# Optimization experiments

Measured on AMD Instinct MI355X. Metric: run time of the kernel, lower is better.

The kernel has to match this reference:

```python
import jax, jax.numpy as jnp
import numpy as np
from jax.scipy.linalg import solve_triangular

DT = 0.1
LOG2PI = float(np.log(2.0 * np.pi))


def _mvn_ll(r, L):
    # r: (B, dz, K) residual, L: (dz, dz) lower-tri Cholesky of cov
    B_, dz, K = r.shape
    y = solve_triangular(L, r.transpose(1, 0, 2).reshape(dz, -1), lower=True)
    quad = jnp.sum(y * y, axis=0).reshape(B_, K)
    logdet = jnp.sum(jnp.log(jnp.diag(L)))
    return -0.5 * quad - logdet - 0.5 * dz * LOG2PI


def _diag_ll(r, std):
    # r: (B, dz, K), std: (dz,) -> (B, K)
    z = r / std[None, :, None]
    return -0.5 * jnp.sum(z * z, axis=1) - jnp.sum(jnp.log(std)) - 0.5 * r.shape[1] * LOG2PI


def _systematic_resample(log_w, key):
    # systematic resampling (aesmc style): stratified positions bucketized into cum weights
    B_, K = log_w.shape
    u0 = jax.random.uniform(key, (B_, 1))
    pos = (u0 + jnp.arange(K, dtype=log_w.dtype)) / K
    w = jax.nn.softmax(jax.lax.stop_gradient(log_w), axis=1)
    cw = jnp.cumsum(w, axis=1)
    cw = cw / cw[:, -1:]
    idx = jax.vmap(lambda c, p: jnp.searchsorted(c, p))(cw, pos)
    return jnp.clip(idx, 0, K - 1)


def _transition(z, v, m, n, Wu, h):
    # low-rank RNN prior: z'= (1-dt) z + dt m^T tanh(n z + Wu v + h); z: (B,dz,K), v: (B,du)
    pre = jnp.einsum('Nz,BzK->BNK', n, z) + (v @ Wu.T)[:, :, None] + h[None, :, None]
    return (1.0 - DT) * z + DT * jnp.einsum('Nz,BNK->BzK', m, jnp.tanh(pre))


def _kalman(var_z, var_x, B_obs):
    # precision-form optimal proposal (dim_x >= 4*dim_z branch)
    dz = var_z.shape[0]
    prec = jnp.diag(1.0 / var_z) + (B_obs / var_x[None, :]) @ B_obs.T
    var_Q = jnp.linalg.inv(prec)
    Kg = var_Q @ (B_obs / var_x[None, :])           # (dz, dx)
    one_min_alpha = jnp.eye(dz) - Kg @ B_obs.T      # (dz, dz)
    var_Q = 1e-8 * jnp.eye(dz) + 0.5 * (var_Q + var_Q.T)
    L = jnp.linalg.cholesky(var_Q)
    return Kg, one_min_alpha, L


def setup_inputs() -> dict:
    key = jax.random.key(0)
    ks = jax.random.split(key, 14)
    B_, dx, T = 128, 128, 512
    dz, du, dN, K = 16, 8, 512, 128
    inp = {
        'x': jax.random.normal(ks[0], (B_, dx, T), jnp.float32),
        'u': jax.random.normal(ks[1], (B_, du, T), jnp.float32),
        'R_z': 0.1 + 0.1 * jax.random.uniform(ks[2], (dz,), jnp.float32),
        'R_z_t0': 0.2 + 0.1 * jax.random.uniform(ks[3], (dz,), jnp.float32),
        'R_x': 0.3 + 0.2 * jax.random.uniform(ks[4], (dx,), jnp.float32),
        'B_obs': jax.random.normal(ks[5], (dz, dx), jnp.float32) / np.sqrt(dz),
        'Obs_bias': 0.1 * jax.random.normal(ks[6], (dx,), jnp.float32),
        'm': jax.random.normal(ks[7], (dN, dz), jnp.float32) / np.sqrt(dN),
        'n': jax.random.normal(ks[8], (dN, dz), jnp.float32) / np.sqrt(dz),
        'Wu': jax.random.normal(ks[9], (dN, du), jnp.float32) / np.sqrt(du),
        'h': 0.1 * jax.random.normal(ks[10], (dN,), jnp.float32),
        'W0': jax.random.normal(ks[11], (dz, du), jnp.float32) / np.sqrt(du),
        'b0': 0.1 * jax.random.normal(ks[12], (dz,), jnp.float32),
        'k': K,
    }
    return inp


def reference(x, u, R_z, R_z_t0, R_x, B_obs, Obs_bias, m, n, Wu, h, W0, b0, k):
    B_, dx, T = x.shape
    dz = R_z.shape[0]
    K = int(k)
    var_z = R_z ** 2 + 1e-8
    var_z0 = R_z_t0 ** 2 + 1e-8
    var_x = jnp.clip(R_x ** 2, 1e-8)
    std_x = jnp.clip(jnp.abs(R_x), 1e-4)
    std_z = jnp.sqrt(var_z)
    std_z0 = jnp.sqrt(var_z0)
    log_std_x_sum = jnp.sum(jnp.log(std_x))

    Kg0, oma0, L0 = _kalman(var_z0, var_x, B_obs)
    Kg, oma, L = _kalman(var_z, var_x, B_obs)
    base = jax.random.key(42)
    logk = jnp.log(jnp.asarray(K, x.dtype))

    def obs_ll(xt, Qz):
        mean_x = jnp.einsum('zx,BzK->BxK', B_obs, Qz) + Obs_bias[None, :, None]
        rx = (xt[:, :, None] - mean_x) / std_x[None, :, None]
        return -0.5 * jnp.sum(rx * rx, axis=1) - log_std_x_sum - 0.5 * dx * LOG2PI

    # t = 0: initial state from stimulus, Kalman optimal proposal
    prior_mean = (u[:, :, 0] @ W0.T + b0)[:, :, None] * jnp.ones((1, 1, K), x.dtype)
    mean_Q = jnp.einsum('zs,BsK->BzK', oma0, prior_mean) \
        + jnp.einsum('zx,Bx->Bz', Kg0, x[:, :, 0] - Obs_bias)[:, :, None]
    eps = jax.random.normal(jax.random.fold_in(base, 0), (B_, dz, K), x.dtype)
    Qz = mean_Q + jnp.einsum('zs,BsK->BzK', L0, eps)
    ll_qz = _mvn_ll(Qz - mean_Q, L0)
    ll_pz = _diag_ll(Qz - prior_mean, std_z0)
    ll_x = obs_ll(x[:, :, 0], Qz)
    log_w = ll_x + ll_pz - ll_qz
    elbo0 = jax.scipy.special.logsumexp(log_w, axis=-1) - logk

    x_tm = jnp.moveaxis(x[:, :, 1:], 2, 0)       # (T-1, B, dx)
    v_tm = jnp.moveaxis(u[:, :, :T - 1], 2, 0)   # v at step t is u[:,:,t-1]
    ts = jnp.arange(1, T)

    def step(carry, inp):
        Qz, log_w = carry
        xt, vt, t = inp
        k1, k2 = jax.random.split(jax.random.fold_in(base, t))
        idx = _systematic_resample(log_w, k1)
        Qz = jnp.take_along_axis(Qz, jnp.broadcast_to(idx[:, None, :], Qz.shape), axis=2)
        prior_mean = _transition(Qz, vt, m, n, Wu, h)
        mean_Q = jnp.einsum('zs,BsK->BzK', oma, prior_mean) \
            + jnp.einsum('zx,Bx->Bz', Kg, xt - Obs_bias)[:, :, None]
        eps = jax.random.normal(k2, Qz.shape, Qz.dtype)
        Qz_new = mean_Q + jnp.einsum('zs,BsK->BzK', L, eps)
        ll_qz = _mvn_ll(Qz_new - mean_Q, L)
        ll_pz = _diag_ll(Qz_new - prior_mean, std_z)
        ll_x = obs_ll(xt, Qz_new)
        log_w_new = ll_x + ll_pz - ll_qz
        return (Qz_new, log_w_new), jax.scipy.special.logsumexp(log_w_new, axis=-1) - logk

    (_, _), elbos = jax.lax.scan(step, (Qz, log_w), (x_tm, v_tm, ts))
    loss = -(elbo0 + jnp.sum(elbos, axis=0)) / T   # (B,) negative per-trial ELBO
    return loss
```

## Files before the change

kernel.cpp:

```cpp
#include <hip/hip_runtime.h>
#include <hip/hip_bf16.h>


#define WS_KG    0
#define WS_OMA   4096
#define WS_L     4608
#define WS_RSTDZ 5120
#define WS_RSTDX 5152
#define WS_CONST 5280

#define LOG2PI_F 1.8378770664093453f

typedef __attribute__((ext_vector_type(8))) short short8v;
typedef __attribute__((ext_vector_type(4))) float float4v;
typedef __attribute__((ext_vector_type(4))) unsigned uint4v;

#define MFMA32(a, b, c) \
  __builtin_amdgcn_mfma_f32_16x16x32_bf16((a), (b), (c), 0, 0, 0)

__device__ __forceinline__ unsigned rotl32(unsigned v, int r) {
  return (v << r) | (v >> (32 - r));
}

__device__ __forceinline__ void tf2x32(unsigned k0, unsigned k1,
                                       unsigned c0, unsigned c1,
                                       unsigned& o0, unsigned& o1) {
  unsigned ks2 = k0 ^ k1 ^ 0x1BD11BDAu;
  unsigned x0 = c0 + k0, x1 = c1 + k1;
#define TF_R4(ra, rb, rc, rd) \
  x0 += x1; x1 = rotl32(x1, ra); x1 ^= x0; \
  x0 += x1; x1 = rotl32(x1, rb); x1 ^= x0; \
  x0 += x1; x1 = rotl32(x1, rc); x1 ^= x0; \
  x0 += x1; x1 = rotl32(x1, rd); x1 ^= x0;
  TF_R4(13, 15, 26, 6)  x0 += k1;  x1 += ks2 + 1u;
  TF_R4(17, 29, 16, 24) x0 += ks2; x1 += k0 + 2u;
  TF_R4(13, 15, 26, 6)  x0 += k0;  x1 += k1 + 3u;
  TF_R4(17, 29, 16, 24) x0 += k1;  x1 += ks2 + 4u;
  TF_R4(13, 15, 26, 6)  x0 += ks2; x1 += k0 + 5u;
#undef TF_R4
  o0 = x0; o1 = x1;
}

__device__ __forceinline__ float erfinv_f(float x) {
  float w = -log1pf(-x * x);
  float p;
  if (w < 5.0f) {
    w -= 2.5f;
    p = 2.81022636e-08f;
    p = fmaf(p, w, 3.43273939e-07f);
    p = fmaf(p, w, -3.5233877e-06f);
    p = fmaf(p, w, -4.39150654e-06f);
    p = fmaf(p, w, 0.00021858087f);
    p = fmaf(p, w, -0.00125372503f);
    p = fmaf(p, w, -0.00417768164f);
    p = fmaf(p, w, 0.246640727f);
    p = fmaf(p, w, 1.50140941f);
  } else {
    w = sqrtf(w) - 3.0f;
    p = -0.000200214257f;
    p = fmaf(p, w, 0.000100950558f);
    p = fmaf(p, w, 0.00134934322f);
    p = fmaf(p, w, -0.00367342844f);
    p = fmaf(p, w, 0.00573950773f);
    p = fmaf(p, w, -0.0076224613f);
    p = fmaf(p, w, 0.00943887047f);
    p = fmaf(p, w, 1.00167406f);
    p = fmaf(p, w, 2.83297682f);
  }
  return p * x;
}

__device__ __forceinline__ float normal_from_bits(unsigned bits) {
  float f = __uint_as_float((bits >> 9) | 0x3f800000u) - 1.0f;
  const float lo = -0.99999994f;
  float uu = fmaxf(lo, fmaf(f, 2.0f, lo));
  return 1.41421354f * erfinv_f(uu);
}

__device__ __forceinline__ float tanh_fast2(float d) {
  float e = __expf(d);
  return 1.0f - 2.0f * __builtin_amdgcn_rcpf(e + 1.0f);
}

__device__ __forceinline__ short f2bf(float f) {
  unsigned u = __float_as_uint(f);
  unsigned r = (u + 0x7fffu + ((u >> 16) & 1u)) >> 16;
  return (short)r;
}

__device__ __forceinline__ unsigned packbf(float a, float b) {
  return (unsigned)(unsigned short)f2bf(a) |
         ((unsigned)(unsigned short)f2bf(b) << 16);
}

__device__ __forceinline__ unsigned cvtpk(float a, float b) {
  unsigned r;
  asm("v_cvt_pk_bf16_f32 %0, %1, %2" : "=v"(r) : "v"(a), "v"(b));
  return r;
}

__device__ __forceinline__ short8v mk8(unsigned a, unsigned b,
                                       unsigned c, unsigned d) {
  uint4v u = {a, b, c, d};
  return __builtin_bit_cast(short8v, u);
}

__global__ void precomp_kernel(const float* __restrict__ Rz,
                               const float* __restrict__ Rz0,
                               const float* __restrict__ Rx,
                               const float* __restrict__ Bobs,
                               float* __restrict__ ws) {
  __shared__ float svarx[128];
  __shared__ float svarz[16];
  __shared__ float sprec[16][16];
  __shared__ float saug[16][32];
  __shared__ float svq[16][16];
  __shared__ float sLm[16][16];
  __shared__ float skg[16][128];
  const int tid = threadIdx.x;

  if (tid < 128) {
    float r = Rx[tid];
    svarx[tid] = fmaxf(r * r, 1e-8f);
    ws[WS_RSTDX + tid] = 1.0f / fmaxf(fabsf(r), 1e-4f);
  }
  if (tid == 0) {
    float a = 0.0f;
    for (int xx = 0; xx < 128; ++xx) a += logf(fmaxf(fabsf(Rx[xx]), 1e-4f));
    ws[WS_CONST + 0] = -a - 0.5f * 128.0f * LOG2PI_F;
  }
  __syncthreads();

  for (int set = 0; set < 2; ++set) {
    const float* Rzp = (set == 0) ? Rz0 : Rz;
    if (tid < 16) {
      float v = Rzp[tid] * Rzp[tid] + 1e-8f;
      svarz[tid] = v;
      ws[WS_RSTDZ + set * 16 + tid] = 1.0f / sqrtf(v);
    }
    __syncthreads();
    {
      int z1 = tid >> 4, z2 = tid & 15;
      float a = 0.0f;
      for (int xx = 0; xx < 128; ++xx)
        a += Bobs[z1 * 128 + xx] * Bobs[z2 * 128 + xx] / svarx[xx];
      if (z1 == z2) a += 1.0f / svarz[z1];
      sprec[z1][z2] = a;
    }
    __syncthreads();
    if (tid == 0) {
      for (int r = 0; r < 16; ++r)
        for (int c2 = 0; c2 < 32; ++c2)
          saug[r][c2] = (c2 < 16) ? sprec[r][c2] : ((c2 - 16 == r) ? 1.0f : 0.0f);
      for (int p = 0; p < 16; ++p) {
        float ip = 1.0f / saug[p][p];
        for (int c2 = 0; c2 < 32; ++c2) saug[p][c2] *= ip;
        for (int r = 0; r < 16; ++r) if (r != p) {
          float f = saug[r][p];
          for (int c2 = 0; c2 < 32; ++c2) saug[r][c2] -= f * saug[p][c2];
        }
      }
      for (int r = 0; r < 16; ++r)
        for (int c2 = 0; c2 < 16; ++c2)
          svq[r][c2] = 0.5f * (saug[r][16 + c2] + saug[c2][16 + r]) +
                       ((r == c2) ? 1e-8f : 0.0f);
      for (int j = 0; j < 16; ++j) {
        float d = svq[j][j];
        for (int s = 0; s < j; ++s) d -= sLm[j][s] * sLm[j][s];
        float dj = sqrtf(d);
        sLm[j][j] = dj;
        for (int r = j + 1; r < 16; ++r) {
          float a = svq[r][j];
          for (int s = 0; s < j; ++s) a -= sLm[r][s] * sLm[j][s];
          sLm[r][j] = a / dj;
        }
        for (int r = 0; r < j; ++r) sLm[r][j] = 0.0f;
      }
      float cc = 0.0f;
      for (int j = 0; j < 16; ++j) cc += logf(sLm[j][j]) - logf(sqrtf(svarz[j]));
      ws[WS_CONST + 1 + set] = cc;
      for (int r = 0; r < 16; ++r)
        for (int c2 = 0; c2 < 16; ++c2)
          ws[WS_L + set * 256 + r * 16 + c2] = sLm[r][c2];
    }
    __syncthreads();
    for (int o = tid; o < 2048; o += 256) {
      int z = o >> 7, xx = o & 127;
      float a = 0.0f;
      for (int s = 0; s < 16; ++s) a += saug[z][16 + s] * Bobs[s * 128 + xx];
      a /= svarx[xx];
      skg[z][xx] = a;
      ws[WS_KG + set * 2048 + o] = a;
    }
    __syncthreads();
    {
      int z = tid >> 4, s = tid & 15;
      float a = 0.0f;
      for (int xx = 0; xx < 128; ++xx) a += skg[z][xx] * Bobs[s * 128 + xx];
      ws[WS_OMA + set * 256 + tid] = ((z == s) ? 1.0f : 0.0f) - a;
    }
    __syncthreads();
  }
}

__global__ __launch_bounds__(512, 1) void pf_kernel(
    const float* __restrict__ xg, const float* __restrict__ ug,
    const float* __restrict__ Bobs, const float* __restrict__ Obias,
    const float* __restrict__ mg, const float* __restrict__ ng,
    const float* __restrict__ Wug, const float* __restrict__ hg,
    const float* __restrict__ W0g, const float* __restrict__ b0g,
    const float* __restrict__ ws, float* __restrict__ out) {
  __shared__ float sPart[8][128][20];
  __shared__ short8v sBF[8][32];
  __shared__ unsigned sKeys[512][4];
  __shared__ __align__(16) unsigned qnA[128 * 12];
  __shared__ __align__(16) unsigned qnB[128 * 12];
  __shared__ __align__(16) unsigned sEB[128 * 12];
  __shared__ __align__(16) float sWV[512];
  __shared__ __align__(16) float sXT[128];
  __shared__ __align__(16) float sXR[128];
  __shared__ __align__(16) float sRX[128];
  __shared__ __align__(16) float sKx[16];
  __shared__ int   sIDX[128];
  __shared__ float sLLC[4][128];
  __shared__ float sLLD[128];
  __shared__ float sLLE[128];

  const int tid  = threadIdx.x;
  const int b    = blockIdx.x;
  const int lane = tid & 63;
  const int wid  = tid >> 6;
  const int q    = lane >> 4;
  const int r16  = lane & 15;

  const short8v zero8 = {0, 0, 0, 0, 0, 0, 0, 0};
  const float4v zero4 = {0.f, 0.f, 0.f, 0.f};

  if (tid < 256) {
    int xt = tid >> 5, sl2 = tid & 31, qq = sl2 >> 4, rr = sl2 & 15;
    short8v v;
#pragma unroll
    for (int i = 0; i < 8; ++i)
      v[i] = f2bf(Bobs[(size_t)(qq * 8 + i) * 128 + xt * 16 + rr]);
    sBF[xt][sl2] = v;
  }
  {
    int t = tid;
    unsigned kt0, kt1;
    tf2x32(0u, 42u, 0u, (unsigned)t, kt0, kt1);
    unsigned k1a = 0, k1b = 0, k2a = kt0, k2b = kt1;
    if (t > 0) {
      tf2x32(kt0, kt1, 0u, 0u, k1a, k1b);
      tf2x32(kt0, kt1, 0u, 1u, k2a, k2b);
    }
    sKeys[t][0] = k1a; sKeys[t][1] = k1b; sKeys[t][2] = k2a; sKeys[t][3] = k2b;
  }
  if (tid < 128) sRX[tid] = ws[WS_RSTDX + tid];

  short8v a1f[4];
#pragma unroll
  for (int j = 0; j < 4; ++j) {
    short8v v = {0, 0, 0, 0, 0, 0, 0, 0};
    const float* src = ng + (size_t)((wid + 8 * j) * 16 + r16) * 16 + 4 * q;
#pragma unroll
    for (int i = 0; i < 4; ++i) v[i] = f2bf(2.0f * src[i]);
    a1f[j] = v;
  }
  short8v a2f[2];
#pragma unroll
  for (int P = 0; P < 2; ++P) {
    short8v v;
#pragma unroll
    for (int i = 0; i < 4; ++i) {
      v[i]     = f2bf(mg[(size_t)((wid + 16 * P) * 16 + 4 * q + i) * 16 + r16]);
      v[4 + i] = f2bf(mg[(size_t)((wid + 16 * P + 8) * 16 + 4 * q + i) * 16 + r16]);
    }
    a2f[P] = v;
  }
  short8v aD;
  {
    const float* adsrc = (q < 2) ? (ws + WS_OMA + 256) : (ws + WS_L + 256);
    const int kb = (q & 1) * 8;
#pragma unroll
    for (int i = 0; i < 8; ++i)
      aD[i] = f2bf(adsrc[r16 * 16 + kb + i]);
  }
  float rsz4[4];
#pragma unroll
  for (int i = 0; i < 4; ++i) rsz4[i] = ws[WS_RSTDZ + 16 + 4 * q + i];

  const float cobs = ws[WS_CONST + 0];
  const float cc0  = ws[WS_CONST + 1];
  const float cc1  = ws[WS_CONST + 2];
  __syncthreads();

  float elbo = 0.0f;
  short* eb16 = (short*)sEB;
  const int p    = wid * 16 + r16;
  const int srcA = 32 * q + r16;
  const int srcB = srcA + 16;
  const int sl   = q * 16 + r16;

  {
    if (wid == 1) {
#pragma unroll
      for (int h2 = 0; h2 < 2; ++h2) {
        int xx = lane + 64 * h2;
        float xv = xg[((size_t)b * 128 + xx) * 512] - Obias[xx];
        sXT[xx] = xv;
        sXR[xx] = xv * sRX[xx];
      }
    }
    {
      unsigned k2a = sKeys[0][2], k2b = sKeys[0][3];
#pragma unroll
      for (int j = 0; j < 2; ++j) {
        int c = tid + 512 * j;
        unsigned o0, o1;
        tf2x32(k2a, k2b, 0u, (unsigned)(b * 2048 + c), o0, o1);
        int f0 = 2 * c, f1 = 2 * c + 1;
        eb16[(f0 & 127) * 24 + (f0 >> 7)] = f2bf(normal_from_bits(o0));
        eb16[(f1 & 127) * 24 + (f1 >> 7)] = f2bf(normal_from_bits(o1));
      }
    }
    __syncthreads();

    {
      const int kk = tid & 127, zg = tid >> 7;
      float ep[16];
#pragma unroll
      for (int w2 = 0; w2 < 8; ++w2) {
        unsigned uw = sEB[kk * 12 + w2];
        ep[2 * w2]     = __uint_as_float(uw << 16);
        ep[2 * w2 + 1] = __uint_as_float(uw & 0xffff0000u);
      }
      float part = 0.0f;
      if (zg == 0) {
        float qd = 0.0f;
#pragma unroll
        for (int s = 0; s < 16; ++s) qd = fmaf(ep[s], ep[s], qd);
        part = 0.5f * qd;
      }
      float v0[8];
#pragma unroll
      for (int d = 0; d < 8; ++d) v0[d] = ug[((size_t)b * 8 + d) * 512];
      float pm0[16];
#pragma unroll
      for (int s = 0; s < 16; ++s) {
        float a = b0g[s];
#pragma unroll
        for (int d = 0; d < 8; ++d) a = fmaf(W0g[s * 8 + d], v0[d], a);
        pm0[s] = a;
      }
      const float* Kg0p = ws + WS_KG;
      const float* omap = ws + WS_OMA;
      const float* Lp   = ws + WS_L;
      const float* rsz  = ws + WS_RSTDZ;
      float qnv[4];
#pragma unroll
      for (int zi = 0; zi < 4; ++zi) {
        int z = zg * 4 + zi;
        float mq = 0.0f;
        for (int xx = 0; xx < 128; ++xx)
          mq = fmaf(Kg0p[z * 128 + xx], sXT[xx], mq);
#pragma unroll
        for (int s = 0; s < 16; ++s) mq = fmaf(omap[z * 16 + s], pm0[s], mq);
        float qn = mq;
#pragma unroll
        for (int s = 0; s < 16; ++s) qn = fmaf(Lp[z * 16 + s], ep[s], qn);
        qnv[zi] = qn;
        float pz = b0g[z];
#pragma unroll
        for (int d = 0; d < 8; ++d) pz = fmaf(W0g[z * 8 + d], v0[d], pz);
        float r = (qn - pz) * rsz[z];
        part = fmaf(-0.5f * r, r, part);
      }
      qnA[kk * 12 + zg * 2 + 0] = packbf(qnv[0], qnv[1]);
      qnA[kk * 12 + zg * 2 + 1] = packbf(qnv[2], qnv[3]);
      sLLC[zg][kk] = part;
    }
    __syncthreads();

    {
      short8v bq = zero8;
      if (q < 2) bq = *(const short8v*)&qnA[p * 12 + q * 4];
      float ea = 0.0f;
#pragma unroll
      for (int xt = 0; xt < 8; ++xt) {
        short8v ab = (q < 2) ? sBF[xt][sl] : zero8;
        float4v d = MFMA32(ab, bq, zero4);
        float4v xr = *(const float4v*)&sXR[xt * 16 + q * 4];
        float4v rx = *(const float4v*)&sRX[xt * 16 + q * 4];
        float d0 = xr.x - d.x * rx.x; ea = fmaf(d0, d0, ea);
        float d1 = xr.y - d.y * rx.y; ea = fmaf(d1, d1, ea);
        float d2 = xr.z - d.z * rx.z; ea = fmaf(d2, d2, ea);
        float d3 = xr.w - d.w * rx.w; ea = fmaf(d3, d3, ea);
      }
      ea += __shfl_xor(ea, 16, 64);
      ea += __shfl_xor(ea, 32, 64);
      if (q == 0) sLLE[p] = ea;
      if (tid < 128)
        sLLD[tid] = sLLC[0][tid] + sLLC[1][tid] + sLLC[2][tid] + sLLC[3][tid];
    }
    __syncthreads();
  }

  for (int t = 1; t < 512; ++t) {
    const unsigned* qnPrev = (t & 1) ? qnA : qnB;
    unsigned* qnCur = (t & 1) ? qnB : qnA;

    if (wid == 0) {
      float cc = (t == 1) ? cc0 : cc1;
      float lw0 = 0, lw1 = 0;
#pragma unroll
      for (int half = 0; half < 2; ++half) {
        int j = 2 * lane + half;
        float v = -0.5f * sLLE[j] + cobs + cc + sLLD[j];
        if (half) lw1 = v; else lw0 = v;
      }
      float mx = fmaxf(lw0, lw1);
#pragma unroll
      for (int d = 32; d >= 1; d >>= 1) mx = fmaxf(mx, __shfl_xor(mx, d, 64));
      float ea = __expf(lw0 - mx), eb = __expf(lw1 - mx);
      float se = ea + eb;
#pragma unroll
      for (int d = 32; d >= 1; d >>= 1) se += __shfl_xor(se, d, 64);
      elbo += logf(se) + mx - 4.85203026f;

      float run = ea + eb;
#pragma unroll
      for (int d = 1; d < 64; d <<= 1) {
        float v = __shfl_up(run, (unsigned)d, 64);
        if (lane >= d) run += v;
      }
      float tot = __shfl(run, 63, 64);
      float inv = 1.0f / tot;
      float c0 = (run - eb) * inv;
      float c1 = run * inv;
      unsigned o0, o1;
      tf2x32(sKeys[t][0], sKeys[t][1], 0u, (unsigned)b, o0, o1);
      unsigned bits = o0 ^ o1;
      float u0 = __uint_as_float((bits >> 9) | 0x3f800000u) - 1.0f;
      int S0, S1;
      {
        int s = (int)fmaf(c0, 128.0f, -u0);
        s = (s < 0) ? 0 : ((s > 128) ? 128 : s);
        while (s > 0   && (u0 + (float)(s - 1)) * 0.0078125f >  c0) --s;
        while (s < 128 && (u0 + (float)s)       * 0.0078125f <= c0) ++s;
        S0 = s;
        s = (int)fmaf(c1, 128.0f, -u0);
        s = (s < 0) ? 0 : ((s > 128) ? 128 : s);
        while (s > 0   && (u0 + (float)(s - 1)) * 0.0078125f >  c1) --s;
        while (s < 128 && (u0 + (float)s)       * 0.0078125f <= c1) ++s;
        S1 = s;
      }
      if (lane == 63) S1 = 128;
      int Sp = __shfl_up(S1, 1, 64);
      if (lane == 0) Sp = 0;
      if (S0 > S1) S0 = S1;
      if (Sp > S0) Sp = S0;
      for (int j = Sp; j < S0; ++j) sIDX[j] = 2 * lane;
      for (int j = S0; j < S1; ++j) sIDX[j] = 2 * lane + 1;
    } else if (wid == 1) {
#pragma unroll
      for (int h2 = 0; h2 < 2; ++h2) {
        int xx = lane + 64 * h2;
        float xv = xg[((size_t)b * 128 + xx) * 512 + t] - Obias[xx];
        sXT[xx] = xv;
        sXR[xx] = xv * sRX[xx];
      }
      int z = lane >> 2, xq = lane & 3;
      const float* Kgp = ws + WS_KG + 2048 + z * 128;
      float a = 0.0f;
      for (int jj = 0; jj < 32; ++jj) {
        int xx = xq + 4 * jj;
        a = fmaf(Kgp[xx], sXT[xx], a);
      }
      a += __shfl_xor(a, 1, 64);
      a += __shfl_xor(a, 2, 64);
      if (xq == 0) sKx[z] = a;
    } else {
      if (wid == 2) {
        float v[8];
#pragma unroll
        for (int d = 0; d < 8; ++d) v[d] = ug[((size_t)b * 8 + d) * 512 + (t - 1)];
#pragma unroll
        for (int qq = 0; qq < 8; ++qq) {
          int N = lane + 64 * qq;
          const float4* wr = (const float4*)&Wug[N * 8];
          float4 wa = wr[0], wb = wr[1];
          float a = hg[N];
          a = fmaf(wa.x, v[0], a); a = fmaf(wa.y, v[1], a);
          a = fmaf(wa.z, v[2], a); a = fmaf(wa.w, v[3], a);
          a = fmaf(wb.x, v[4], a); a = fmaf(wb.y, v[5], a);
          a = fmaf(wb.z, v[6], a); a = fmaf(wb.w, v[7], a);
          sWV[N] = 2.0f * a;
        }
      }
      unsigned k2a = sKeys[t][2], k2b = sKeys[t][3];
      int lt = tid - 128;
      for (int c = lt; c < 1024; c += 384) {
        unsigned o0, o1;
        tf2x32(k2a, k2b, 0u, (unsigned)(b * 2048 + c), o0, o1);
        int f0 = 2 * c, f1 = 2 * c + 1;
        eb16[(f0 & 127) * 24 + (f0 >> 7)] = f2bf(normal_from_bits(o0));
        eb16[(f1 & 127) * 24 + (f1 >> 7)] = f2bf(normal_from_bits(o1));
      }
    }
    __syncthreads();

    {
      float4v cin[4];
#pragma unroll
      for (int j = 0; j < 4; ++j)
        cin[j] = *(const float4v*)&sWV[(wid + 8 * j) * 16 + 4 * q];
      uint2 zw8[8];
#pragma unroll
      for (int pt = 0; pt < 8; ++pt) {
        int idxp = sIDX[pt * 16 + r16];
        zw8[pt] = *(const uint2*)&qnPrev[idxp * 12 + 2 * q];
      }
#pragma unroll
      for (int pt = 0; pt < 8; ++pt) {
        const int pp = pt * 16 + r16;
        short8v bz = mk8(zw8[pt].x, zw8[pt].y, 0u, 0u);
        float4v d1a = MFMA32(a1f[0], bz, cin[0]);
        float4v d1b = MFMA32(a1f[1], bz, cin[1]);
        float4v d1c = MFMA32(a1f[2], bz, cin[2]);
        float4v d1d = MFMA32(a1f[3], bz, cin[3]);
        unsigned pa0 = cvtpk(tanh_fast2(d1a.x), tanh_fast2(d1a.y));
        unsigned pa1 = cvtpk(tanh_fast2(d1a.z), tanh_fast2(d1a.w));
        unsigned pb0 = cvtpk(tanh_fast2(d1b.x), tanh_fast2(d1b.y));
        unsigned pb1 = cvtpk(tanh_fast2(d1b.z), tanh_fast2(d1b.w));
        unsigned pc0 = cvtpk(tanh_fast2(d1c.x), tanh_fast2(d1c.y));
        unsigned pc1 = cvtpk(tanh_fast2(d1c.z), tanh_fast2(d1c.w));
        unsigned pd0 = cvtpk(tanh_fast2(d1d.x), tanh_fast2(d1d.y));
        unsigned pd1 = cvtpk(tanh_fast2(d1d.z), tanh_fast2(d1d.w));
        float4v a8 = MFMA32(a2f[0], mk8(pa0, pa1, pb0, pb1), zero4);
        a8 = MFMA32(a2f[1], mk8(pc0, pc1, pd0, pd1), a8);
        *(float4v*)&sPart[wid][pp][4 * q] = a8;
      }
    }
    __syncthreads();

    {
      float4v red = zero4;
#pragma unroll
      for (int wv = 0; wv < 8; ++wv)
        red += *(const float4v*)&sPart[wv][p][4 * q];
      const int idxp = sIDX[p];
      uint2 zw = *(const uint2*)&qnPrev[idxp * 12 + 2 * q];
      float zl0 = __uint_as_float(zw.x << 16);
      float zl1 = __uint_as_float(zw.x & 0xffff0000u);
      float zl2 = __uint_as_float(zw.y << 16);
      float zl3 = __uint_as_float(zw.y & 0xffff0000u);
      float pm0 = fmaf(0.1f, red.x, 0.9f * zl0);
      float pm1 = fmaf(0.1f, red.y, 0.9f * zl1);
      float pm2 = fmaf(0.1f, red.z, 0.9f * zl2);
      float pm3 = fmaf(0.1f, red.w, 0.9f * zl3);

      unsigned w01 = cvtpk(pm0, pm1), w23 = cvtpk(pm2, pm3);
      unsigned bA0 = (unsigned)__shfl((int)w01, srcA, 64);
      unsigned bA1 = (unsigned)__shfl((int)w23, srcA, 64);
      unsigned bB0 = (unsigned)__shfl((int)w01, srcB, 64);
      unsigned bB1 = (unsigned)__shfl((int)w23, srcB, 64);
      short8v bw;
      if (q < 2) {
        uint4v uu = {bA0, bA1, bB0, bB1};
        bw = __builtin_bit_cast(short8v, uu);
      } else {
        bw = *(const short8v*)&sEB[p * 12 + (q - 2) * 4];
      }
      float4v cinD = *(const float4v*)&sKx[4 * q];
      float4v aq = MFMA32(aD, bw, cinD);
      float part = 0.0f;
      if (q >= 2) {
        uint4v uw = __builtin_bit_cast(uint4v, bw);
        float e0 = __uint_as_float(uw.x << 16);
        float e1 = __uint_as_float(uw.x & 0xffff0000u);
        float e2 = __uint_as_float(uw.y << 16);
        float e3 = __uint_as_float(uw.y & 0xffff0000u);
        float e4 = __uint_as_float(uw.z << 16);
        float e5 = __uint_as_float(uw.z & 0xffff0000u);
        float e6 = __uint_as_float(uw.w << 16);
        float e7 = __uint_as_float(uw.w & 0xffff0000u);
        float s2 = 0.0f;
        s2 = fmaf(e0, e0, s2); s2 = fmaf(e1, e1, s2);
        s2 = fmaf(e2, e2, s2); s2 = fmaf(e3, e3, s2);
        s2 = fmaf(e4, e4, s2); s2 = fmaf(e5, e5, s2);
        s2 = fmaf(e6, e6, s2); s2 = fmaf(e7, e7, s2);
        part = 0.5f * s2;
      }
      float r0 = (aq.x - pm0) * rsz4[0];
      float r1 = (aq.y - pm1) * rsz4[1];
      float r2 = (aq.z - pm2) * rsz4[2];
      float r3 = (aq.w - pm3) * rsz4[3];
      part = fmaf(-0.5f * r0, r0, part);
      part = fmaf(-0.5f * r1, r1, part);
      part = fmaf(-0.5f * r2, r2, part);
      part = fmaf(-0.5f * r3, r3, part);
      unsigned y01 = cvtpk(aq.x, aq.y), y23 = cvtpk(aq.z, aq.w);
      *(uint2*)&qnCur[p * 12 + 2 * q] = make_uint2(y01, y23);
      part += __shfl_xor(part, 16, 64);
      part += __shfl_xor(part, 32, 64);
      if (q == 0) sLLD[p] = part;

      unsigned qA0 = (unsigned)__shfl((int)y01, srcA, 64);
      unsigned qA1 = (unsigned)__shfl((int)y23, srcA, 64);
      unsigned qB0 = (unsigned)__shfl((int)y01, srcB, 64);
      unsigned qB1 = (unsigned)__shfl((int)y23, srcB, 64);
      short8v bq = zero8;
      if (q < 2) {
        uint4v uu = {qA0, qA1, qB0, qB1};
        bq = __builtin_bit_cast(short8v, uu);
      }
      float ea = 0.0f;
#pragma unroll
      for (int xt = 0; xt < 8; ++xt) {
        short8v ab = (q < 2) ? sBF[xt][sl] : zero8;
        float4v d = MFMA32(ab, bq, zero4);
        float4v xr = *(const float4v*)&sXR[xt * 16 + q * 4];
        float4v rx = *(const float4v*)&sRX[xt * 16 + q * 4];
        float d0 = xr.x - d.x * rx.x; ea = fmaf(d0, d0, ea);
        float d1 = xr.y - d.y * rx.y; ea = fmaf(d1, d1, ea);
        float d2 = xr.z - d.z * rx.z; ea = fmaf(d2, d2, ea);
        float d3 = xr.w - d.w * rx.w; ea = fmaf(d3, d3, ea);
      }
      ea += __shfl_xor(ea, 16, 64);
      ea += __shfl_xor(ea, 32, 64);
      if (q == 0) sLLE[p] = ea;
    }
    __syncthreads();
  }

  if (wid == 0) {
    float lw0 = 0, lw1 = 0;
#pragma unroll
    for (int half = 0; half < 2; ++half) {
      int j = 2 * lane + half;
      float v = -0.5f * sLLE[j] + cobs + cc1 + sLLD[j];
      if (half) lw1 = v; else lw0 = v;
    }
    float mx = fmaxf(lw0, lw1);
#pragma unroll
    for (int d = 32; d >= 1; d >>= 1) mx = fmaxf(mx, __shfl_xor(mx, d, 64));
    float se = __expf(lw0 - mx) + __expf(lw1 - mx);
#pragma unroll
    for (int d = 32; d >= 1; d >>= 1) se += __shfl_xor(se, d, 64);
    elbo += logf(se) + mx - 4.85203026f;
  }
  if (tid == 0) out[b] = -elbo * (1.0f / 512.0f);
}

extern "C" void kernel_launch(void* const* d_in, const int* in_sizes, int n_in,
                              void* d_out, int out_size, void* d_ws, size_t ws_size,
                              hipStream_t stream) {
  const float* x     = (const float*)d_in[0];
  const float* u     = (const float*)d_in[1];
  const float* R_z   = (const float*)d_in[2];
  const float* R_z0  = (const float*)d_in[3];
  const float* R_x   = (const float*)d_in[4];
  const float* B_obs = (const float*)d_in[5];
  const float* Obias = (const float*)d_in[6];
  const float* m     = (const float*)d_in[7];
  const float* n     = (const float*)d_in[8];
  const float* Wu    = (const float*)d_in[9];
  const float* h     = (const float*)d_in[10];
  const float* W0    = (const float*)d_in[11];
  const float* b0    = (const float*)d_in[12];
  float* ws = (float*)d_ws;
  float* outp = (float*)d_out;

  precomp_kernel<<<dim3(1), dim3(256), 0, stream>>>(R_z, R_z0, R_x, B_obs, ws);
  pf_kernel<<<dim3(128), dim3(512), 0, stream>>>(x, u, B_obs, Obias, m, n, Wu, h,
                                                 W0, b0, ws, outp);
}
```

Baseline: 4.815 ms.

## Double-buffer noise generation one step ahead and fold log2e into tanh

The Gaussian noise buffer becomes double-buffered. Noise for step t+1 is now generated by all threads after the first barrier of step t, instead of by waves 1-7 during the resampling phase, so the RNG work spreads across the whole block. The 2*log2(e) factor is pre-folded into the n weights and the Wu·v bias so tanh can use exp2 in place of exp. This adds more LDS and puts RNG work into the transition phase, which may lengthen that phase.

```diff
diff --git a/kernel.cpp b/kernel.cpp
--- a/kernel.cpp
+++ b/kernel.cpp
@@ -10,6 +10,7 @@
 #define WS_CONST 5280
 
 #define LOG2PI_F 1.8378770664093453f
+#define TWO_LOG2E 2.8853900817779268f
 
 typedef __attribute__((ext_vector_type(8))) short short8v;
 typedef __attribute__((ext_vector_type(4))) float float4v;
@@ -77,8 +78,8 @@
   return 1.41421354f * erfinv_f(uu);
 }
 
-__device__ __forceinline__ float tanh_fast2(float d) {
-  float e = __expf(d);
+__device__ __forceinline__ float tanh_fast2e(float d) {
+  float e = exp2f(d);
   return 1.0f - 2.0f * __builtin_amdgcn_rcpf(e + 1.0f);
 }
 
@@ -215,7 +216,7 @@
   __shared__ unsigned sKeys[512][4];
   __shared__ __align__(16) unsigned qnA[128 * 12];
   __shared__ __align__(16) unsigned qnB[128 * 12];
-  __shared__ __align__(16) unsigned sEB[128 * 12];
+  __shared__ __align__(16) unsigned sEB[2][128 * 12];
   __shared__ __align__(16) float sWV[512];
   __shared__ __align__(16) float sXT[128];
   __shared__ __align__(16) float sXR[128];
@@ -263,7 +264,7 @@
     short8v v = {0, 0, 0, 0, 0, 0, 0, 0};
     const float* src = ng + (size_t)((wid + 8 * j) * 16 + r16) * 16 + 4 * q;
 #pragma unroll
-    for (int i = 0; i < 4; ++i) v[i] = f2bf(2.0f * src[i]);
+    for (int i = 0; i < 4; ++i) v[i] = f2bf(TWO_LOG2E * src[i]);
     a1f[j] = v;
   }
   short8v a2f[2];
@@ -295,7 +296,6 @@
   __syncthreads();
 
   float elbo = 0.0f;
-  short* eb16 = (short*)sEB;
   const int p    = wid * 16 + r16;
   const int srcA = 32 * q + r16;
   const int srcB = srcA + 16;
@@ -312,15 +312,19 @@
       }
     }
     {
-      unsigned k2a = sKeys[0][2], k2b = sKeys[0][3];
-#pragma unroll
-      for (int j = 0; j < 2; ++j) {
-        int c = tid + 512 * j;
-        unsigned o0, o1;
-        tf2x32(k2a, k2b, 0u, (unsigned)(b * 2048 + c), o0, o1);
-        int f0 = 2 * c, f1 = 2 * c + 1;
-        eb16[(f0 & 127) * 24 + (f0 >> 7)] = f2bf(normal_from_bits(o0));
-        eb16[(f1 & 127) * 24 + (f1 >> 7)] = f2bf(normal_from_bits(o1));
+#pragma unroll
+      for (int st = 0; st < 2; ++st) {
+        short* ebw = (short*)sEB[st];
+        unsigned k2a = sKeys[st][2], k2b = sKeys[st][3];
+#pragma unroll
+        for (int j = 0; j < 2; ++j) {
+          int c = tid + 512 * j;
+          unsigned o0, o1;
+          tf2x32(k2a, k2b, 0u, (unsigned)(b * 2048 + c), o0, o1);
+          int f0 = 2 * c, f1 = 2 * c + 1;
+          ebw[(f0 & 127) * 24 + (f0 >> 7)] = f2bf(normal_from_bits(o0));
+          ebw[(f1 & 127) * 24 + (f1 >> 7)] = f2bf(normal_from_bits(o1));
+        }
       }
     }
     __syncthreads();
@@ -330,7 +334,7 @@
       float ep[16];
 #pragma unroll
       for (int w2 = 0; w2 < 8; ++w2) {
-        unsigned uw = sEB[kk * 12 + w2];
+        unsigned uw = sEB[0][kk * 12 + w2];
         ep[2 * w2]     = __uint_as_float(uw << 16);
         ep[2 * w2 + 1] = __uint_as_float(uw & 0xffff0000u);
       }
@@ -408,6 +412,7 @@
   for (int t = 1; t < 512; ++t) {
     const unsigned* qnPrev = (t & 1) ? qnA : qnB;
     unsigned* qnCur = (t & 1) ? qnB : qnA;
+    const unsigned* ebR = sEB[t & 1];
 
     if (wid == 0) {
       float cc = (t == 1) ? cc0 : cc1;
@@ -479,37 +484,39 @@
       a += __shfl_xor(a, 1, 64);
       a += __shfl_xor(a, 2, 64);
       if (xq == 0) sKx[z] = a;
-    } else {
-      if (wid == 2) {
-        float v[8];
-#pragma unroll
-        for (int d = 0; d < 8; ++d) v[d] = ug[((size_t)b * 8 + d) * 512 + (t - 1)];
-#pragma unroll
-        for (int qq = 0; qq < 8; ++qq) {
-          int N = lane + 64 * qq;
-          const float4* wr = (const float4*)&Wug[N * 8];
-          float4 wa = wr[0], wb = wr[1];
-          float a = hg[N];
-          a = fmaf(wa.x, v[0], a); a = fmaf(wa.y, v[1], a);
-          a = fmaf(wa.z, v[2], a); a = fmaf(wa.w, v[3], a);
-          a = fmaf(wb.x, v[4], a); a = fmaf(wb.y, v[5], a);
-          a = fmaf(wb.z, v[6], a); a = fmaf(wb.w, v[7], a);
-          sWV[N] = 2.0f * a;
+    } else if (wid == 2) {
+      float v[8];
+#pragma unroll
+      for (int d = 0; d < 8; ++d) v[d] = ug[((size_t)b * 8 + d) * 512 + (t - 1)];
+#pragma unroll
+      for (int qq = 0; qq < 8; ++qq) {
+        int N = lane + 64 * qq;
+        const float4* wr = (const float4*)&Wug[N * 8];
+        float4 wa = wr[0], wb = wr[1];
+        float a = hg[N];
+        a = fmaf(wa.x, v[0], a); a = fmaf(wa.y, v[1], a);
+        a = fmaf(wa.z, v[2], a); a = fmaf(wa.w, v[3], a);
+        a = fmaf(wb.x, v[4], a); a = fmaf(wb.y, v[5], a);
+        a = fmaf(wb.z, v[6], a); a = fmaf(wb.w, v[7], a);
+        sWV[N] = TWO_LOG2E * a;
+      }
+    }
+    __syncthreads();
+
+    {
+      if (t < 511) {
+        short* ebw = (short*)sEB[(t + 1) & 1];
+        unsigned k2a = sKeys[t + 1][2], k2b = sKeys[t + 1][3];
+#pragma unroll
+        for (int j = 0; j < 2; ++j) {
+          int c = tid + 512 * j;
+          unsigned o0, o1;
+          tf2x32(k2a, k2b, 0u, (unsigned)(b * 2048 + c), o0, o1);
+          int f0 = 2 * c, f1 = 2 * c + 1;
+          ebw[(f0 & 127) * 24 + (f0 >> 7)] = f2bf(normal_from_bits(o0));
+          ebw[(f1 & 127) * 24 + (f1 >> 7)] = f2bf(normal_from_bits(o1));
         }
       }
-      unsigned k2a = sKeys[t][2], k2b = sKeys[t][3];
-      int lt = tid - 128;
-      for (int c = lt; c < 1024; c += 384) {
-        unsigned o0, o1;
-        tf2x32(k2a, k2b, 0u, (unsigned)(b * 2048 + c), o0, o1);
-        int f0 = 2 * c, f1 = 2 * c + 1;
-        eb16[(f0 & 127) * 24 + (f0 >> 7)] = f2bf(normal_from_bits(o0));
-        eb16[(f1 & 127) * 24 + (f1 >> 7)] = f2bf(normal_from_bits(o1));
-      }
-    }
-    __syncthreads();
-
-    {
       float4v cin[4];
 #pragma unroll
       for (int j = 0; j < 4; ++j)
@@ -528,14 +535,14 @@
         float4v d1b = MFMA32(a1f[1], bz, cin[1]);
         float4v d1c = MFMA32(a1f[2], bz, cin[2]);
         float4v d1d = MFMA32(a1f[3], bz, cin[3]);
-        unsigned pa0 = cvtpk(tanh_fast2(d1a.x), tanh_fast2(d1a.y));
-        unsigned pa1 = cvtpk(tanh_fast2(d1a.z), tanh_fast2(d1a.w));
-        unsigned pb0 = cvtpk(tanh_fast2(d1b.x), tanh_fast2(d1b.y));
-        unsigned pb1 = cvtpk(tanh_fast2(d1b.z), tanh_fast2(d1b.w));
-        unsigned pc0 = cvtpk(tanh_fast2(d1c.x), tanh_fast2(d1c.y));
-        unsigned pc1 = cvtpk(tanh_fast2(d1c.z), tanh_fast2(d1c.w));
-        unsigned pd0 = cvtpk(tanh_fast2(d1d.x), tanh_fast2(d1d.y));
-        unsigned pd1 = cvtpk(tanh_fast2(d1d.z), tanh_fast2(d1d.w));
+        unsigned pa0 = cvtpk(tanh_fast2e(d1a.x), tanh_fast2e(d1a.y));
+        unsigned pa1 = cvtpk(tanh_fast2e(d1a.z), tanh_fast2e(d1a.w));
+        unsigned pb0 = cvtpk(tanh_fast2e(d1b.x), tanh_fast2e(d1b.y));
+        unsigned pb1 = cvtpk(tanh_fast2e(d1b.z), tanh_fast2e(d1b.w));
+        unsigned pc0 = cvtpk(tanh_fast2e(d1c.x), tanh_fast2e(d1c.y));
+        unsigned pc1 = cvtpk(tanh_fast2e(d1c.z), tanh_fast2e(d1c.w));
+        unsigned pd0 = cvtpk(tanh_fast2e(d1d.x), tanh_fast2e(d1d.y));
+        unsigned pd1 = cvtpk(tanh_fast2e(d1d.z), tanh_fast2e(d1d.w));
         float4v a8 = MFMA32(a2f[0], mk8(pa0, pa1, pb0, pb1), zero4);
         a8 = MFMA32(a2f[1], mk8(pc0, pc1, pd0, pd1), a8);
         *(float4v*)&sPart[wid][pp][4 * q] = a8;
@@ -569,7 +576,7 @@
         uint4v uu = {bA0, bA1, bB0, bB1};
         bw = __builtin_bit_cast(short8v, uu);
       } else {
-        bw = *(const short8v*)&sEB[p * 12 + (q - 2) * 4];
+        bw = *(const short8v*)&ebR[p * 12 + (q - 2) * 4];
       }
       float4v cinD = *(const float4v*)&sKx[4 * q];
       float4v aq = MFMA32(aD, bw, cinD);
```

New measurement: 6.335 ms. 1.32x slower.
